# Kernel tuning notes

Measured on AMD Instinct MI355X. Metric: run time of the kernel, lower is better.

The kernel has to match this reference:

```python
import jax, jax.numpy as jnp
import numpy as np

B, T, D = 2, 2048, 1024
H, KVH = 16, 4
HD = D // H            # 64
HALF = HD // 2         # 32
DFF = 4096
KW = 15
EPS = 1e-6


def zcrms(x, scale):
    # zero-centred RMSNorm: (1 + scale) * x / rms(x)
    rms = jnp.sqrt(jnp.mean(jnp.square(x.astype(jnp.float32)), axis=-1, keepdims=True) + EPS)
    return ((1.0 + scale) * x / rms).astype(x.dtype)


def apply_rope(x, cos, sin):
    # x: [B, H, T, HD]; cos/sin: [T, HALF]
    c = cos[None, None, :, :]
    s = sin[None, None, :, :]
    x1, x2 = x[..., :HALF], x[..., HALF:]
    return jnp.concatenate([x1 * c - x2 * s, x2 * c + x1 * s], axis=-1)


def setup_inputs() -> dict:
    key = jax.random.key(0)
    ks = jax.random.split(key, 20)
    std = 0.02
    inp = {
        "x": jax.random.normal(ks[0], (B, T, D), jnp.float32),
        "mask": jnp.ones((1, 1, T, T), dtype=bool),
        "cos": jnp.cos(jnp.arange(T, dtype=jnp.float32)[:, None]
                       * (10000.0 ** (-jnp.arange(HALF, dtype=jnp.float32) / HALF))[None, :]),
        "sin": jnp.sin(jnp.arange(T, dtype=jnp.float32)[:, None]
                       * (10000.0 ** (-jnp.arange(HALF, dtype=jnp.float32) / HALF))[None, :]),
        # attention
        "attn_norm_scale": jax.random.normal(ks[1], (D,), jnp.float32) * std,
        "q_kernel": jax.random.normal(ks[2], (D, D), jnp.float32) * std,
        "k_kernel": jax.random.normal(ks[3], (D, KVH * HD), jnp.float32) * std,
        "v_kernel": jax.random.normal(ks[4], (D, KVH * HD), jnp.float32) * std,
        "q_norm_scale": jax.random.normal(ks[5], (HD,), jnp.float32) * std,
        "k_norm_scale": jax.random.normal(ks[6], (HD,), jnp.float32) * std,
        "o_kernel": jax.random.normal(ks[7], (D, D), jnp.float32) * std,
        # conv module
        "conv_norm_scale": jax.random.normal(ks[8], (D,), jnp.float32) * std,
        "pw_up_kernel": jax.random.normal(ks[9], (D, 2 * D), jnp.float32) * std,
        "dw_kernel": jax.random.normal(ks[10], (KW, 1, D), jnp.float32) * std,
        "conv_inner_norm_scale": jax.random.normal(ks[11], (D,), jnp.float32) * std,
        "pw_down_kernel": jax.random.normal(ks[12], (D, D), jnp.float32) * std,
        # ffn
        "ffn_norm_scale": jax.random.normal(ks[13], (D,), jnp.float32) * std,
        "gate_kernel": jax.random.normal(ks[14], (D, DFF), jnp.float32) * std,
        "up_kernel": jax.random.normal(ks[15], (D, DFF), jnp.float32) * std,
        "down_kernel": jax.random.normal(ks[16], (DFF, D), jnp.float32) * std,
    }
    return inp


def reference(x, mask, cos, sin, attn_norm_scale, q_kernel, k_kernel, v_kernel,
              q_norm_scale, k_norm_scale, o_kernel, conv_norm_scale, pw_up_kernel,
              dw_kernel, conv_inner_norm_scale, pw_down_kernel, ffn_norm_scale,
              gate_kernel, up_kernel, down_kernel):
    # ---- pre-norm self-attention (GQA + QK-RMSNorm + RoPE) ----
    h = zcrms(x, attn_norm_scale)
    q = (h @ q_kernel).reshape(B, T, H, HD).transpose(0, 2, 1, 3)      # [B,H,T,HD]
    k = (h @ k_kernel).reshape(B, T, KVH, HD).transpose(0, 2, 1, 3)    # [B,KVH,T,HD]
    v = (h @ v_kernel).reshape(B, T, KVH, HD).transpose(0, 2, 1, 3)
    q = zcrms(q, q_norm_scale)
    k = zcrms(k, k_norm_scale)
    rep = H // KVH
    k = jnp.repeat(k, rep, axis=1)
    v = jnp.repeat(v, rep, axis=1)
    q = apply_rope(q, cos, sin)
    k = apply_rope(k, cos, sin)
    scale = jnp.sqrt(jnp.float32(HD))
    aw = jnp.einsum('bhqd,bhkd->bhqk', q, k) / scale
    aw = jnp.where(mask, aw, jnp.finfo(aw.dtype).min)
    aw = jax.nn.softmax(aw, axis=-1)
    attn = jnp.einsum('bhqk,bhkd->bhqd', aw, v).transpose(0, 2, 1, 3).reshape(B, T, D)
    x = x + attn @ o_kernel

    # ---- conformer conv module: pw_up -> GLU -> depthwise conv -> norm -> pw_down ----
    h = zcrms(x, conv_norm_scale)
    u = h @ pw_up_kernel
    u1, u2 = jnp.split(u, 2, axis=-1)
    g = u1 * jax.nn.sigmoid(u2)                                        # [B,T,D]
    c = jax.lax.conv_general_dilated(
        g, dw_kernel, window_strides=(1,), padding='SAME',
        feature_group_count=D, dimension_numbers=('NWC', 'WIO', 'NWC'))
    c = zcrms(c, conv_inner_norm_scale)
    x = x + c @ pw_down_kernel

    # ---- gated FFN with drelu activation ----
    h = zcrms(x, ffn_norm_scale)
    ff = jax.nn.relu(h @ gate_kernel) * jax.nn.relu(h @ up_kernel)
    x = x + ff @ down_kernel
    return x
```

## Files before the change

kernel.cpp:

```cpp
#include <hip/hip_runtime.h>


#define TT   2048
#define NTOK 4096

typedef __attribute__((ext_vector_type(8))) short short8;
typedef __attribute__((ext_vector_type(4))) float floatx4;

__device__ __forceinline__ unsigned short f2bf(float f) {
  unsigned int u = __float_as_uint(f);
  u = (u + 0x7fffu + ((u >> 16) & 1u)) >> 16;
  return (unsigned short)u;
}
__device__ __forceinline__ float bf2f(unsigned short s) {
  return __uint_as_float(((unsigned int)s) << 16);
}

__device__ __forceinline__ void glds16(const void* g, void* lds_base) {
  __builtin_amdgcn_global_load_lds(
      (const __attribute__((address_space(1))) void*)g,
      (__attribute__((address_space(3))) void*)lds_base, 16, 0, 0);
}

__global__ void wconv_kernel(const float* __restrict__ src,
                             unsigned short* __restrict__ dst, int K, int M) {
  __shared__ float tile[32][33];
  int m0 = blockIdx.x * 32, k0 = blockIdx.y * 32;
  int tx = threadIdx.x, ty = threadIdx.y;
  for (int j = ty; j < 32; j += 8)
    tile[j][tx] = src[(size_t)(k0 + j) * M + (m0 + tx)];
  __syncthreads();
  for (int j = ty; j < 32; j += 8)
    dst[(size_t)(m0 + j) * K + (k0 + tx)] = f2bf(tile[tx][j]);
}

__global__ __launch_bounds__(256) void rmsnorm_kernel(
    const float* __restrict__ x, const float* __restrict__ scale,
    unsigned short* __restrict__ out) {
  int t = blockIdx.x, tid = threadIdx.x;
  float4 xv = ((const float4*)(x + (size_t)t * 1024))[tid];
  float ss = xv.x * xv.x + xv.y * xv.y + xv.z * xv.z + xv.w * xv.w;
#pragma unroll
  for (int off = 32; off > 0; off >>= 1) ss += __shfl_down(ss, off);
  __shared__ float red[4];
  if ((tid & 63) == 0) red[tid >> 6] = ss;
  __syncthreads();
  float rinv = rsqrtf((red[0] + red[1] + red[2] + red[3]) * (1.0f / 1024.0f) + 1e-6f);
  float4 sv = ((const float4*)scale)[tid];
  ushort4 o;
  o.x = f2bf((1.0f + sv.x) * xv.x * rinv);
  o.y = f2bf((1.0f + sv.y) * xv.y * rinv);
  o.z = f2bf((1.0f + sv.z) * xv.z * rinv);
  o.w = f2bf((1.0f + sv.w) * xv.w * rinv);
  ((ushort4*)(out + (size_t)t * 1024))[tid] = o;
}

template <int BN, bool OUT_BF16, bool RELU, bool RESID>
__global__ __launch_bounds__(256, 2) void gemm_bt_kernel(
    const unsigned short* __restrict__ A, const unsigned short* __restrict__ Bt,
    void* __restrict__ Cout, const float* __restrict__ resid, int K, int M) {
  constexpr int NI = BN / 32;
  __shared__ __align__(16) unsigned short As[128 * 64];
  __shared__ __align__(16) unsigned short Bs[BN * 64];
  const int tid = threadIdx.x;
  const int wid = tid >> 6, lane = tid & 63;
  const int quad = lane >> 4, l16 = lane & 15;
  const int wm = (wid >> 1) * 64, wn = (wid & 1) * (BN / 2);
  const int row0 = blockIdx.y * 128;
  const int col0 = blockIdx.x * BN;

  floatx4 acc[4][NI];
#pragma unroll
  for (int mi = 0; mi < 4; mi++)
#pragma unroll
    for (int ni = 0; ni < NI; ni++) acc[mi][ni] = (floatx4){0.f, 0.f, 0.f, 0.f};

  const unsigned short* Ag = A + (size_t)row0 * K;
  const unsigned short* Bg = Bt + (size_t)col0 * K;

  for (int k0 = 0; k0 < K; k0 += 64) {
#pragma unroll
    for (int j = 0; j < 4; j++) {
      int ci = tid + j * 256;
      int r = ci >> 3, c = (ci & 7) ^ (r & 7);
      glds16(Ag + (size_t)r * K + k0 + c * 8, &As[(wid * 64 + j * 256) * 8]);
    }
#pragma unroll
    for (int j = 0; j < BN / 32; j++) {
      int ci = tid + j * 256;
      int r = ci >> 3, c = (ci & 7) ^ (r & 7);
      glds16(Bg + (size_t)r * K + k0 + c * 8, &Bs[(wid * 64 + j * 256) * 8]);
    }
    __syncthreads();
#pragma unroll
    for (int kk = 0; kk < 64; kk += 32) {
      short8 a[4], b[NI];
#pragma unroll
      for (int mi = 0; mi < 4; mi++) {
        int r = wm + mi * 16 + l16;
        a[mi] = *(const short8*)&As[r * 64 + (((kk >> 3) + quad) ^ (r & 7)) * 8];
      }
#pragma unroll
      for (int ni = 0; ni < NI; ni++) {
        int r = wn + ni * 16 + l16;
        b[ni] = *(const short8*)&Bs[r * 64 + (((kk >> 3) + quad) ^ (r & 7)) * 8];
      }
#pragma unroll
      for (int mi = 0; mi < 4; mi++)
#pragma unroll
        for (int ni = 0; ni < NI; ni++)
          acc[mi][ni] = __builtin_amdgcn_mfma_f32_16x16x32_bf16(a[mi], b[ni], acc[mi][ni], 0, 0, 0);
    }
    __syncthreads();
  }
#pragma unroll
  for (int mi = 0; mi < 4; mi++) {
#pragma unroll
    for (int reg = 0; reg < 4; reg++) {
      int grow = row0 + wm + mi * 16 + quad * 4 + reg;
#pragma unroll
      for (int ni = 0; ni < NI; ni++) {
        int gcol = col0 + wn + ni * 16 + l16;
        float v = acc[mi][ni][reg];
        if (RESID) v += resid[(size_t)grow * M + gcol];
        if (RELU) v = fmaxf(v, 0.f);
        if (OUT_BF16) ((unsigned short*)Cout)[(size_t)grow * M + gcol] = f2bf(v);
        else          ((float*)Cout)[(size_t)grow * M + gcol] = v;
      }
    }
  }
}

#define QSCALE 0.180336880111f

__global__ __launch_bounds__(256) void qknorm_rope_kernel(
    const float* __restrict__ qkv, const float* __restrict__ cosb,
    const float* __restrict__ sinb, const float* __restrict__ qns,
    const float* __restrict__ kns, unsigned short* __restrict__ qb,
    unsigned short* __restrict__ kb, unsigned short* __restrict__ vb) {
  int tok = blockIdx.x;
  int tid = threadIdx.x, w = tid >> 6, lane = tid & 63;
  int pos = tok & (TT - 1);
  int half = lane & 31;
  float c = cosb[pos * 32 + half], s = sinb[pos * 32 + half];
  const float* row = qkv + (size_t)tok * 1536;
  for (int hr = w; hr < 20; hr += 4) {
    float v = row[hr * 64 + lane];
    float ss = v * v;
#pragma unroll
    for (int off = 32; off > 0; off >>= 1) ss += __shfl_xor(ss, off);
    float rinv = rsqrtf(ss * (1.0f / 64.0f) + 1e-6f);
    float sc = (hr < 16) ? qns[lane] : kns[lane];
    float nv = (1.0f + sc) * v * rinv;
    float partner = __shfl_xor(nv, 32);
    float outv = (lane < 32) ? (nv * c - partner * s) : (nv * c + partner * s);
    if (hr < 16) qb[(size_t)tok * 1024 + hr * 64 + lane] = f2bf(outv * QSCALE);
    else         kb[(size_t)tok * 256 + (hr - 16) * 64 + lane] = f2bf(outv);
  }
  vb[(size_t)tok * 256 + tid] = f2bf(row[1280 + tid]);
}

__global__ __launch_bounds__(256) void flash_kernel(
    const unsigned short* __restrict__ qb, const unsigned short* __restrict__ kb,
    const unsigned short* __restrict__ vb, unsigned short* __restrict__ ob) {
  int qt = blockIdx.x;
  int bh = blockIdx.y;
  int bi = bh >> 4, h = bh & 15, kvh = h >> 2;
  int tid = threadIdx.x, w = tid >> 6, lane = tid & 63;
  int quad = lane >> 4, l16 = lane & 15;

  __shared__ __align__(16) unsigned short Ks[2][64 * 64];
  __shared__ __align__(16) unsigned short Vt[2][64 * 72];
  __shared__ __align__(16) unsigned short Ps[64 * 76];

  const unsigned short* qsrc = qb + ((size_t)(bi * TT + qt * 64)) * 1024 + h * 64;
  short8 qf0 = *(const short8*)(qsrc + (size_t)(w * 16 + l16) * 1024 + quad * 8);
  short8 qf1 = *(const short8*)(qsrc + (size_t)(w * 16 + l16) * 1024 + 32 + quad * 8);

  const unsigned short* kbase = kb + ((size_t)(bi * TT)) * 256 + kvh * 64;
  const unsigned short* vbase = vb + ((size_t)(bi * TT)) * 256 + kvh * 64;

  floatx4 oacc[4];
  floatx4 lacc = (floatx4){0.f, 0.f, 0.f, 0.f};
#pragma unroll
  for (int i = 0; i < 4; i++) oacc[i] = (floatx4){0.f, 0.f, 0.f, 0.f};
  const short8 ones = (short8){0x3F80, 0x3F80, 0x3F80, 0x3F80,
                               0x3F80, 0x3F80, 0x3F80, 0x3F80};

  const int vkey = tid & 63, vd0 = (tid >> 6) * 8;

#pragma unroll
  for (int j = 0; j < 2; j++) {
    int ci = tid + j * 256;
    int r = ci >> 3, c = (ci & 7) ^ (r & 7);
    glds16(kbase + (size_t)r * 256 + c * 8, &Ks[0][(w * 64 + j * 256) * 8]);
  }
  {
    uint4 t0 = *(const uint4*)(vbase + (size_t)vkey * 256 + vd0);
    uint4 t1 = *(const uint4*)(vbase + (size_t)vkey * 256 + vd0 + 32);
    union { uint4 v; unsigned short u[8]; } uu;
    uu.v = t0;
#pragma unroll
    for (int e = 0; e < 8; e++) Vt[0][(vd0 + e) * 72 + vkey] = uu.u[e];
    uu.v = t1;
#pragma unroll
    for (int e = 0; e < 8; e++) Vt[0][(vd0 + 32 + e) * 72 + vkey] = uu.u[e];
  }

  for (int kt = 0; kt < 32; kt++) {
    const int bufi = kt & 1;
    __syncthreads();
    uint4 n0 = {0, 0, 0, 0}, n1 = {0, 0, 0, 0};
    if (kt < 31) {
#pragma unroll
      for (int j = 0; j < 2; j++) {
        int ci = tid + j * 256;
        int r = ci >> 3, c = (ci & 7) ^ (r & 7);
        glds16(kbase + (size_t)((kt + 1) * 64 + r) * 256 + c * 8,
               &Ks[bufi ^ 1][(w * 64 + j * 256) * 8]);
      }
      n0 = *(const uint4*)(vbase + (size_t)((kt + 1) * 64 + vkey) * 256 + vd0);
      n1 = *(const uint4*)(vbase + (size_t)((kt + 1) * 64 + vkey) * 256 + vd0 + 32);
    }

    float p[4][4];
#pragma unroll
    for (int ni = 0; ni < 4; ni++) {
      int rb = ni * 16 + l16;
      short8 b0 = *(const short8*)&Ks[bufi][rb * 64 + (quad ^ (rb & 7)) * 8];
      short8 b1 = *(const short8*)&Ks[bufi][rb * 64 + ((4 + quad) ^ (rb & 7)) * 8];
      floatx4 s = (floatx4){0.f, 0.f, 0.f, 0.f};
      s = __builtin_amdgcn_mfma_f32_16x16x32_bf16(qf0, b0, s, 0, 0, 0);
      s = __builtin_amdgcn_mfma_f32_16x16x32_bf16(qf1, b1, s, 0, 0, 0);
#pragma unroll
      for (int r = 0; r < 4; r++) p[ni][r] = __builtin_amdgcn_exp2f(s[r]);
    }
#pragma unroll
    for (int ni = 0; ni < 4; ni++)
#pragma unroll
      for (int r = 0; r < 4; r++)
        Ps[(w * 16 + quad * 4 + r) * 76 + ni * 16 + l16] =
            (unsigned short)(__float_as_uint(p[ni][r]) >> 16);
    short8 pa0 = *(const short8*)&Ps[(w * 16 + l16) * 76 + quad * 8];
    short8 pa1 = *(const short8*)&Ps[(w * 16 + l16) * 76 + 32 + quad * 8];
    lacc = __builtin_amdgcn_mfma_f32_16x16x32_bf16(pa0, ones, lacc, 0, 0, 0);
    lacc = __builtin_amdgcn_mfma_f32_16x16x32_bf16(pa1, ones, lacc, 0, 0, 0);
#pragma unroll
    for (int di = 0; di < 4; di++) {
      short8 b0 = *(const short8*)&Vt[bufi][(di * 16 + l16) * 72 + quad * 8];
      short8 b1 = *(const short8*)&Vt[bufi][(di * 16 + l16) * 72 + 32 + quad * 8];
      oacc[di] = __builtin_amdgcn_mfma_f32_16x16x32_bf16(pa0, b0, oacc[di], 0, 0, 0);
      oacc[di] = __builtin_amdgcn_mfma_f32_16x16x32_bf16(pa1, b1, oacc[di], 0, 0, 0);
    }

    if (kt < 31) {
      union { uint4 v; unsigned short u[8]; } uu;
      uu.v = n0;
#pragma unroll
      for (int e = 0; e < 8; e++) Vt[bufi ^ 1][(vd0 + e) * 72 + vkey] = uu.u[e];
      uu.v = n1;
#pragma unroll
      for (int e = 0; e < 8; e++) Vt[bufi ^ 1][(vd0 + 32 + e) * 72 + vkey] = uu.u[e];
    }
  }

  unsigned short* obase = ob + ((size_t)(bi * TT + qt * 64)) * 1024 + h * 64;
  float rl[4];
#pragma unroll
  for (int r = 0; r < 4; r++) rl[r] = 1.0f / lacc[r];
#pragma unroll
  for (int di = 0; di < 4; di++)
#pragma unroll
    for (int r = 0; r < 4; r++) {
      int qrow = w * 16 + quad * 4 + r;
      obase[(size_t)qrow * 1024 + di * 16 + l16] = f2bf(oacc[di][r] * rl[r]);
    }
}

__global__ __launch_bounds__(256) void glu_kernel(const float* __restrict__ u,
                                                  unsigned short* __restrict__ g) {
  int idx = blockIdx.x * 256 + threadIdx.x;
  int t = idx >> 8, c4 = (idx & 255) * 4;
  float4 a = *(const float4*)(u + (size_t)t * 2048 + c4);
  float4 b = *(const float4*)(u + (size_t)t * 2048 + 1024 + c4);
  ushort4 o;
  o.x = f2bf(a.x / (1.0f + __expf(-b.x)));
  o.y = f2bf(a.y / (1.0f + __expf(-b.y)));
  o.z = f2bf(a.z / (1.0f + __expf(-b.z)));
  o.w = f2bf(a.w / (1.0f + __expf(-b.w)));
  *(ushort4*)(g + (size_t)t * 1024 + c4) = o;
}

__global__ __launch_bounds__(256) void convnorm_kernel(
    const unsigned short* __restrict__ g, const float* __restrict__ dw,
    const float* __restrict__ scale, unsigned short* __restrict__ out) {
  int tok = blockIdx.x;
  int bi = tok >> 11, pos = tok & (TT - 1);
  int tid = threadIdx.x, c0 = tid * 4;
  float a0 = 0.f, a1 = 0.f, a2 = 0.f, a3 = 0.f;
#pragma unroll
  for (int wk = 0; wk < 15; wk++) {
    int pp = pos + wk - 7;
    if (pp < 0 || pp >= TT) continue;
    ushort4 gv = *(const ushort4*)(g + ((size_t)(bi * TT + pp)) * 1024 + c0);
    float4 kv = *(const float4*)(dw + wk * 1024 + c0);
    a0 += bf2f(gv.x) * kv.x;
    a1 += bf2f(gv.y) * kv.y;
    a2 += bf2f(gv.z) * kv.z;
    a3 += bf2f(gv.w) * kv.w;
  }
  float ss = a0 * a0 + a1 * a1 + a2 * a2 + a3 * a3;
#pragma unroll
  for (int off = 32; off > 0; off >>= 1) ss += __shfl_down(ss, off);
  __shared__ float red[4];
  if ((tid & 63) == 0) red[tid >> 6] = ss;
  __syncthreads();
  float rinv = rsqrtf((red[0] + red[1] + red[2] + red[3]) * (1.0f / 1024.0f) + 1e-6f);
  float4 sv = *(const float4*)(scale + c0);
  ushort4 o;
  o.x = f2bf((1.0f + sv.x) * a0 * rinv);
  o.y = f2bf((1.0f + sv.y) * a1 * rinv);
  o.z = f2bf((1.0f + sv.z) * a2 * rinv);
  o.w = f2bf((1.0f + sv.w) * a3 * rinv);
  *(ushort4*)(out + (size_t)tok * 1024 + c0) = o;
}

__global__ __launch_bounds__(256) void ffmul_kernel(
    const unsigned short* __restrict__ gu, unsigned short* __restrict__ ff) {
  int idx = blockIdx.x * 256 + threadIdx.x;
  int t = idx >> 10, c4 = (idx & 1023) * 4;
  ushort4 a = *(const ushort4*)(gu + (size_t)t * 8192 + c4);
  ushort4 b = *(const ushort4*)(gu + (size_t)t * 8192 + 4096 + c4);
  ushort4 o;
  o.x = f2bf(bf2f(a.x) * bf2f(b.x));
  o.y = f2bf(bf2f(a.y) * bf2f(b.y));
  o.z = f2bf(bf2f(a.z) * bf2f(b.z));
  o.w = f2bf(bf2f(a.w) * bf2f(b.w));
  *(ushort4*)(ff + (size_t)t * 4096 + c4) = o;
}

extern "C" void kernel_launch(void* const* d_in, const int* in_sizes, int n_in,
                              void* d_out, int out_size, void* d_ws, size_t ws_size,
                              hipStream_t stream) {
  const float* x        = (const float*)d_in[0];
  const float* cosb     = (const float*)d_in[2];
  const float* sinb     = (const float*)d_in[3];
  const float* attn_ns  = (const float*)d_in[4];
  const float* qkern    = (const float*)d_in[5];
  const float* kkern    = (const float*)d_in[6];
  const float* vkern    = (const float*)d_in[7];
  const float* qns      = (const float*)d_in[8];
  const float* kns      = (const float*)d_in[9];
  const float* okern    = (const float*)d_in[10];
  const float* conv_ns  = (const float*)d_in[11];
  const float* pwupk    = (const float*)d_in[12];
  const float* dwk      = (const float*)d_in[13];
  const float* convi_ns = (const float*)d_in[14];
  const float* pwdnk    = (const float*)d_in[15];
  const float* ffn_ns   = (const float*)d_in[16];
  const float* gatek    = (const float*)d_in[17];
  const float* upk      = (const float*)d_in[18];
  const float* downk    = (const float*)d_in[19];
  float* out = (float*)d_out;
  char* ws = (char*)d_ws;

  const size_t O_QKVT = 0;
  const size_t O_OT   = O_QKVT + (size_t)1536 * 1024 * 2;
  const size_t O_UPT  = O_OT   + (size_t)1024 * 1024 * 2;
  const size_t O_DNT  = O_UPT  + (size_t)2048 * 1024 * 2;
  const size_t O_GUT  = O_DNT  + (size_t)1024 * 1024 * 2;
  const size_t O_DWNT = O_GUT  + (size_t)8192 * 1024 * 2;
  const size_t O_H    = O_DWNT + (size_t)4096 * 1024 * 2;
  const size_t O_BIG1 = O_H    + (size_t)4096 * 1024 * 2;
  const size_t O_QB   = O_BIG1 + (size_t)4096 * 8192 * 2;
  const size_t O_KB   = O_QB   + (size_t)4096 * 1024 * 2;
  const size_t O_VB   = O_KB   + (size_t)4096 * 256 * 2;
  const size_t O_ECN  = O_VB   + (size_t)4096 * 256 * 2;
  const size_t O_X1   = O_ECN  + (size_t)4096 * 1024 * 2;
  const size_t O_X2   = O_X1   + (size_t)4096 * 1024 * 4;
  const size_t O_BIG2 = O_X2   + (size_t)4096 * 1024 * 4;

  unsigned short* qkvT = (unsigned short*)(ws + O_QKVT);
  unsigned short* oT   = (unsigned short*)(ws + O_OT);
  unsigned short* upT  = (unsigned short*)(ws + O_UPT);
  unsigned short* dnT  = (unsigned short*)(ws + O_DNT);
  unsigned short* guT  = (unsigned short*)(ws + O_GUT);
  unsigned short* dwT  = (unsigned short*)(ws + O_DWNT);
  unsigned short* hbuf = (unsigned short*)(ws + O_H);
  float*          big1f = (float*)(ws + O_BIG1);
  unsigned short* big1u = (unsigned short*)(ws + O_BIG1);
  unsigned short* qbuf = (unsigned short*)(ws + O_QB);
  unsigned short* kbuf = (unsigned short*)(ws + O_KB);
  unsigned short* vbuf = (unsigned short*)(ws + O_VB);
  unsigned short* ecn  = (unsigned short*)(ws + O_ECN);
  float*          x1   = (float*)(ws + O_X1);
  float*          x2   = (float*)(ws + O_X2);
  unsigned short* big2 = (unsigned short*)(ws + O_BIG2);

  dim3 tb(32, 8);
  wconv_kernel<<<dim3(32, 32), tb, 0, stream>>>(qkern, qkvT, 1024, 1024);
  wconv_kernel<<<dim3(8, 32), tb, 0, stream>>>(kkern, qkvT + (size_t)1024 * 1024, 1024, 256);
  wconv_kernel<<<dim3(8, 32), tb, 0, stream>>>(vkern, qkvT + (size_t)1280 * 1024, 1024, 256);
  wconv_kernel<<<dim3(32, 32), tb, 0, stream>>>(okern, oT, 1024, 1024);
  wconv_kernel<<<dim3(64, 32), tb, 0, stream>>>(pwupk, upT, 1024, 2048);
  wconv_kernel<<<dim3(32, 32), tb, 0, stream>>>(pwdnk, dnT, 1024, 1024);
  wconv_kernel<<<dim3(128, 32), tb, 0, stream>>>(gatek, guT, 1024, 4096);
  wconv_kernel<<<dim3(128, 32), tb, 0, stream>>>(upk, guT + (size_t)4096 * 1024, 1024, 4096);
  wconv_kernel<<<dim3(32, 128), tb, 0, stream>>>(downk, dwT, 4096, 1024);

  rmsnorm_kernel<<<NTOK, 256, 0, stream>>>(x, attn_ns, hbuf);
  gemm_bt_kernel<128, false, false, false><<<dim3(12, 32), 256, 0, stream>>>(
      hbuf, qkvT, big1f, nullptr, 1024, 1536);
  qknorm_rope_kernel<<<NTOK, 256, 0, stream>>>(big1f, cosb, sinb, qns, kns,
                                               qbuf, kbuf, vbuf);
  flash_kernel<<<dim3(32, 32), 256, 0, stream>>>(qbuf, kbuf, vbuf, ecn);
  gemm_bt_kernel<64, false, false, true><<<dim3(16, 32), 256, 0, stream>>>(
      ecn, oT, x1, x, 1024, 1024);

  rmsnorm_kernel<<<NTOK, 256, 0, stream>>>(x1, conv_ns, hbuf);
  gemm_bt_kernel<128, false, false, false><<<dim3(16, 32), 256, 0, stream>>>(
      hbuf, upT, big1f, nullptr, 1024, 2048);
  glu_kernel<<<4096, 256, 0, stream>>>(big1f, big2);
  convnorm_kernel<<<NTOK, 256, 0, stream>>>(big2, dwk, convi_ns, ecn);
  gemm_bt_kernel<64, false, false, true><<<dim3(16, 32), 256, 0, stream>>>(
      ecn, dnT, x2, x1, 1024, 1024);

  rmsnorm_kernel<<<NTOK, 256, 0, stream>>>(x2, ffn_ns, hbuf);
  gemm_bt_kernel<128, true, true, false><<<dim3(64, 32), 256, 0, stream>>>(
      hbuf, guT, big1u, nullptr, 1024, 8192);
  ffmul_kernel<<<16384, 256, 0, stream>>>(big1u, big2);
  gemm_bt_kernel<64, false, false, true><<<dim3(16, 32), 256, 0, stream>>>(
      big2, dwT, out, x2, 4096, 1024);
}
```

Measured before the change: 565.3 us.

## Batch weight conversions into one launch and restructure flash attention tiling

All nine weight transpose-and-convert launches are merged into a single kernel that reads a job table, cutting launch overhead. V is pre-transposed into a separate buffer by a new kernel, so flash attention can load V tiles straight into LDS with async swizzled copies instead of scattering through registers each iteration. Each flash block now handles 128 query rows (32 per wave), reusing every K/V tile across two MFMA row fragments, with a swizzled P buffer. The costs are an extra transpose kernel, more workspace, and half as many flash blocks (512), which may lower occupancy.

```diff
diff --git a/kernel.cpp b/kernel.cpp
--- a/kernel.cpp
+++ b/kernel.cpp
@@ -22,16 +22,30 @@
       (__attribute__((address_space(3))) void*)lds_base, 16, 0, 0);
 }
 
-__global__ void wconv_kernel(const float* __restrict__ src,
-                             unsigned short* __restrict__ dst, int K, int M) {
+struct WJobs {
+  const float* src[9];
+  unsigned short* dst[9];
+  int K[9], M[9];
+  int start[10];
+};
+
+__global__ __launch_bounds__(256) void wconv_all_kernel(WJobs tab) {
+  int b = blockIdx.x;
+  int j = 0;
+  while (b >= tab.start[j + 1]) j++;
+  int t = b - tab.start[j];
+  const float* src = tab.src[j];
+  unsigned short* dst = tab.dst[j];
+  int K = tab.K[j], M = tab.M[j];
+  int mt = M >> 5;
+  int m0 = (t % mt) * 32, k0 = (t / mt) * 32;
   __shared__ float tile[32][33];
-  int m0 = blockIdx.x * 32, k0 = blockIdx.y * 32;
-  int tx = threadIdx.x, ty = threadIdx.y;
-  for (int j = ty; j < 32; j += 8)
-    tile[j][tx] = src[(size_t)(k0 + j) * M + (m0 + tx)];
+  int tx = threadIdx.x & 31, ty = threadIdx.x >> 5;
+  for (int r = ty; r < 32; r += 8)
+    tile[r][tx] = src[(size_t)(k0 + r) * M + m0 + tx];
   __syncthreads();
-  for (int j = ty; j < 32; j += 8)
-    dst[(size_t)(m0 + j) * K + (k0 + tx)] = f2bf(tile[tx][j]);
+  for (int r = ty; r < 32; r += 8)
+    dst[(size_t)(m0 + r) * K + k0 + tx] = f2bf(tile[tx][r]);
 }
 
 __global__ __launch_bounds__(256) void rmsnorm_kernel(
@@ -160,121 +174,150 @@
   vb[(size_t)tok * 256 + tid] = f2bf(row[1280 + tid]);
 }
 
+__global__ __launch_bounds__(256) void vtrans_kernel(
+    const unsigned short* __restrict__ vb, unsigned short* __restrict__ vt) {
+  __shared__ unsigned short t[64 * 65];
+  int ktile = blockIdx.x;
+  int g = blockIdx.y;
+  int bi = g >> 2, kvh = g & 3;
+  int tid = threadIdx.x;
+#pragma unroll
+  for (int j = 0; j < 2; j++) {
+    int ci = tid + j * 256;
+    int r = ci >> 3, c8 = (ci & 7) * 8;
+    union { uint4 v; unsigned short u[8]; } uu;
+    uu.v = *(const uint4*)(vb + (size_t)(bi * TT + ktile * 64 + r) * 256 + kvh * 64 + c8);
+#pragma unroll
+    for (int e = 0; e < 8; e++) t[r * 65 + c8 + e] = uu.u[e];
+  }
+  __syncthreads();
+#pragma unroll
+  for (int j = 0; j < 2; j++) {
+    int ci = tid + j * 256;
+    int d = ci >> 3, c8 = (ci & 7) * 8;
+    union { uint4 v; unsigned short u[8]; } uu;
+#pragma unroll
+    for (int e = 0; e < 8; e++) uu.u[e] = t[(c8 + e) * 65 + d];
+    *(uint4*)(vt + ((size_t)(g * 64 + d)) * TT + ktile * 64 + c8) = uu.v;
+  }
+}
+
 __global__ __launch_bounds__(256) void flash_kernel(
     const unsigned short* __restrict__ qb, const unsigned short* __restrict__ kb,
-    const unsigned short* __restrict__ vb, unsigned short* __restrict__ ob) {
-  int qt = blockIdx.x;
-  int bh = blockIdx.y;
-  int bi = bh >> 4, h = bh & 15, kvh = h >> 2;
-  int tid = threadIdx.x, w = tid >> 6, lane = tid & 63;
-  int quad = lane >> 4, l16 = lane & 15;
+    const unsigned short* __restrict__ vt, unsigned short* __restrict__ ob) {
+  const int qt = blockIdx.x;
+  const int bh = blockIdx.y;
+  const int bi = bh >> 4, h = bh & 15, kvh = h >> 2;
+  const int tid = threadIdx.x, w = tid >> 6, lane = tid & 63;
+  const int quad = lane >> 4, l16 = lane & 15;
 
   __shared__ __align__(16) unsigned short Ks[2][64 * 64];
-  __shared__ __align__(16) unsigned short Vt[2][64 * 72];
-  __shared__ __align__(16) unsigned short Ps[64 * 76];
-
-  const unsigned short* qsrc = qb + ((size_t)(bi * TT + qt * 64)) * 1024 + h * 64;
-  short8 qf0 = *(const short8*)(qsrc + (size_t)(w * 16 + l16) * 1024 + quad * 8);
-  short8 qf1 = *(const short8*)(qsrc + (size_t)(w * 16 + l16) * 1024 + 32 + quad * 8);
+  __shared__ __align__(16) unsigned short Vs[2][64 * 64];
+  __shared__ __align__(16) unsigned short Ps[128 * 72];
+
+  const unsigned short* qsrc = qb + ((size_t)(bi * TT + qt * 128)) * 1024 + h * 64;
+  short8 qf[2][2];
+#pragma unroll
+  for (int af = 0; af < 2; af++) {
+    const unsigned short* qr = qsrc + (size_t)(w * 32 + af * 16 + l16) * 1024;
+    qf[af][0] = *(const short8*)(qr + quad * 8);
+    qf[af][1] = *(const short8*)(qr + 32 + quad * 8);
+  }
 
   const unsigned short* kbase = kb + ((size_t)(bi * TT)) * 256 + kvh * 64;
-  const unsigned short* vbase = vb + ((size_t)(bi * TT)) * 256 + kvh * 64;
-
-  floatx4 oacc[4];
-  floatx4 lacc = (floatx4){0.f, 0.f, 0.f, 0.f};
-#pragma unroll
-  for (int i = 0; i < 4; i++) oacc[i] = (floatx4){0.f, 0.f, 0.f, 0.f};
+  const unsigned short* vbase = vt + ((size_t)(bi * 4 + kvh)) * (64 * TT);
+
+  floatx4 oacc[2][4];
+  floatx4 lacc[2];
+#pragma unroll
+  for (int af = 0; af < 2; af++) {
+    lacc[af] = (floatx4){0.f, 0.f, 0.f, 0.f};
+#pragma unroll
+    for (int di = 0; di < 4; di++) oacc[af][di] = (floatx4){0.f, 0.f, 0.f, 0.f};
+  }
   const short8 ones = (short8){0x3F80, 0x3F80, 0x3F80, 0x3F80,
                                0x3F80, 0x3F80, 0x3F80, 0x3F80};
-
-  const int vkey = tid & 63, vd0 = (tid >> 6) * 8;
 
 #pragma unroll
   for (int j = 0; j < 2; j++) {
     int ci = tid + j * 256;
     int r = ci >> 3, c = (ci & 7) ^ (r & 7);
     glds16(kbase + (size_t)r * 256 + c * 8, &Ks[0][(w * 64 + j * 256) * 8]);
-  }
-  {
-    uint4 t0 = *(const uint4*)(vbase + (size_t)vkey * 256 + vd0);
-    uint4 t1 = *(const uint4*)(vbase + (size_t)vkey * 256 + vd0 + 32);
-    union { uint4 v; unsigned short u[8]; } uu;
-    uu.v = t0;
-#pragma unroll
-    for (int e = 0; e < 8; e++) Vt[0][(vd0 + e) * 72 + vkey] = uu.u[e];
-    uu.v = t1;
-#pragma unroll
-    for (int e = 0; e < 8; e++) Vt[0][(vd0 + 32 + e) * 72 + vkey] = uu.u[e];
+    glds16(vbase + (size_t)r * TT + c * 8, &Vs[0][(w * 64 + j * 256) * 8]);
   }
 
   for (int kt = 0; kt < 32; kt++) {
-    const int bufi = kt & 1;
+    const int buf = kt & 1;
     __syncthreads();
-    uint4 n0 = {0, 0, 0, 0}, n1 = {0, 0, 0, 0};
     if (kt < 31) {
 #pragma unroll
       for (int j = 0; j < 2; j++) {
         int ci = tid + j * 256;
         int r = ci >> 3, c = (ci & 7) ^ (r & 7);
         glds16(kbase + (size_t)((kt + 1) * 64 + r) * 256 + c * 8,
-               &Ks[bufi ^ 1][(w * 64 + j * 256) * 8]);
-      }
-      n0 = *(const uint4*)(vbase + (size_t)((kt + 1) * 64 + vkey) * 256 + vd0);
-      n1 = *(const uint4*)(vbase + (size_t)((kt + 1) * 64 + vkey) * 256 + vd0 + 32);
-    }
-
-    float p[4][4];
+               &Ks[buf ^ 1][(w * 64 + j * 256) * 8]);
+        glds16(vbase + (size_t)r * TT + (kt + 1) * 64 + c * 8,
+               &Vs[buf ^ 1][(w * 64 + j * 256) * 8]);
+      }
+    }
+
+    short8 kf[4][2];
 #pragma unroll
     for (int ni = 0; ni < 4; ni++) {
       int rb = ni * 16 + l16;
-      short8 b0 = *(const short8*)&Ks[bufi][rb * 64 + (quad ^ (rb & 7)) * 8];
-      short8 b1 = *(const short8*)&Ks[bufi][rb * 64 + ((4 + quad) ^ (rb & 7)) * 8];
-      floatx4 s = (floatx4){0.f, 0.f, 0.f, 0.f};
-      s = __builtin_amdgcn_mfma_f32_16x16x32_bf16(qf0, b0, s, 0, 0, 0);
-      s = __builtin_amdgcn_mfma_f32_16x16x32_bf16(qf1, b1, s, 0, 0, 0);
-#pragma unroll
-      for (int r = 0; r < 4; r++) p[ni][r] = __builtin_amdgcn_exp2f(s[r]);
-    }
-#pragma unroll
-    for (int ni = 0; ni < 4; ni++)
-#pragma unroll
-      for (int r = 0; r < 4; r++)
-        Ps[(w * 16 + quad * 4 + r) * 76 + ni * 16 + l16] =
-            (unsigned short)(__float_as_uint(p[ni][r]) >> 16);
-    short8 pa0 = *(const short8*)&Ps[(w * 16 + l16) * 76 + quad * 8];
-    short8 pa1 = *(const short8*)&Ps[(w * 16 + l16) * 76 + 32 + quad * 8];
-    lacc = __builtin_amdgcn_mfma_f32_16x16x32_bf16(pa0, ones, lacc, 0, 0, 0);
-    lacc = __builtin_amdgcn_mfma_f32_16x16x32_bf16(pa1, ones, lacc, 0, 0, 0);
+      kf[ni][0] = *(const short8*)&Ks[buf][rb * 64 + ((quad ^ (rb & 7)) * 8)];
+      kf[ni][1] = *(const short8*)&Ks[buf][rb * 64 + (((4 + quad) ^ (rb & 7)) * 8)];
+    }
+#pragma unroll
+    for (int af = 0; af < 2; af++) {
+#pragma unroll
+      for (int ni = 0; ni < 4; ni++) {
+        floatx4 s = (floatx4){0.f, 0.f, 0.f, 0.f};
+        s = __builtin_amdgcn_mfma_f32_16x16x32_bf16(qf[af][0], kf[ni][0], s, 0, 0, 0);
+        s = __builtin_amdgcn_mfma_f32_16x16x32_bf16(qf[af][1], kf[ni][1], s, 0, 0, 0);
+#pragma unroll
+        for (int r = 0; r < 4; r++)
+          Ps[(w * 32 + af * 16 + quad * 4 + r) * 72 + ((ni ^ quad) * 16 + l16)] =
+              (unsigned short)(__float_as_uint(__builtin_amdgcn_exp2f(s[r])) >> 16);
+      }
+    }
+    short8 vf[4][2];
 #pragma unroll
     for (int di = 0; di < 4; di++) {
-      short8 b0 = *(const short8*)&Vt[bufi][(di * 16 + l16) * 72 + quad * 8];
-      short8 b1 = *(const short8*)&Vt[bufi][(di * 16 + l16) * 72 + 32 + quad * 8];
-      oacc[di] = __builtin_amdgcn_mfma_f32_16x16x32_bf16(pa0, b0, oacc[di], 0, 0, 0);
-      oacc[di] = __builtin_amdgcn_mfma_f32_16x16x32_bf16(pa1, b1, oacc[di], 0, 0, 0);
-    }
-
-    if (kt < 31) {
-      union { uint4 v; unsigned short u[8]; } uu;
-      uu.v = n0;
-#pragma unroll
-      for (int e = 0; e < 8; e++) Vt[bufi ^ 1][(vd0 + e) * 72 + vkey] = uu.u[e];
-      uu.v = n1;
-#pragma unroll
-      for (int e = 0; e < 8; e++) Vt[bufi ^ 1][(vd0 + 32 + e) * 72 + vkey] = uu.u[e];
-    }
-  }
-
-  unsigned short* obase = ob + ((size_t)(bi * TT + qt * 64)) * 1024 + h * 64;
-  float rl[4];
-#pragma unroll
-  for (int r = 0; r < 4; r++) rl[r] = 1.0f / lacc[r];
-#pragma unroll
-  for (int di = 0; di < 4; di++)
-#pragma unroll
-    for (int r = 0; r < 4; r++) {
-      int qrow = w * 16 + quad * 4 + r;
-      obase[(size_t)qrow * 1024 + di * 16 + l16] = f2bf(oacc[di][r] * rl[r]);
-    }
+      int rb = di * 16 + l16;
+      vf[di][0] = *(const short8*)&Vs[buf][rb * 64 + ((quad ^ (rb & 7)) * 8)];
+      vf[di][1] = *(const short8*)&Vs[buf][rb * 64 + (((4 + quad) ^ (rb & 7)) * 8)];
+    }
+#pragma unroll
+    for (int af = 0; af < 2; af++) {
+      const int rr = w * 32 + af * 16 + l16;
+      const int sw = l16 >> 2;
+      short8 pa0 = *(const short8*)&Ps[rr * 72 + (((quad >> 1) ^ sw) * 16 + (quad & 1) * 8)];
+      short8 pa1 = *(const short8*)&Ps[rr * 72 + ((((quad >> 1) + 2) ^ sw) * 16 + (quad & 1) * 8)];
+      lacc[af] = __builtin_amdgcn_mfma_f32_16x16x32_bf16(pa0, ones, lacc[af], 0, 0, 0);
+      lacc[af] = __builtin_amdgcn_mfma_f32_16x16x32_bf16(pa1, ones, lacc[af], 0, 0, 0);
+#pragma unroll
+      for (int di = 0; di < 4; di++) {
+        oacc[af][di] = __builtin_amdgcn_mfma_f32_16x16x32_bf16(pa0, vf[di][0], oacc[af][di], 0, 0, 0);
+        oacc[af][di] = __builtin_amdgcn_mfma_f32_16x16x32_bf16(pa1, vf[di][1], oacc[af][di], 0, 0, 0);
+      }
+    }
+  }
+
+  unsigned short* obase = ob + ((size_t)(bi * TT + qt * 128)) * 1024 + h * 64;
+#pragma unroll
+  for (int af = 0; af < 2; af++) {
+    float rl[4];
+#pragma unroll
+    for (int r = 0; r < 4; r++) rl[r] = 1.0f / lacc[af][r];
+#pragma unroll
+    for (int di = 0; di < 4; di++)
+#pragma unroll
+      for (int r = 0; r < 4; r++) {
+        int qrow = w * 32 + af * 16 + quad * 4 + r;
+        obase[(size_t)qrow * 1024 + di * 16 + l16] = f2bf(oacc[af][di][r] * rl[r]);
+      }
+  }
 }
 
 __global__ __launch_bounds__(256) void glu_kernel(const float* __restrict__ u,
@@ -375,7 +418,8 @@
   const size_t O_QB   = O_BIG1 + (size_t)4096 * 8192 * 2;
   const size_t O_KB   = O_QB   + (size_t)4096 * 1024 * 2;
   const size_t O_VB   = O_KB   + (size_t)4096 * 256 * 2;
-  const size_t O_ECN  = O_VB   + (size_t)4096 * 256 * 2;
+  const size_t O_VT   = O_VB   + (size_t)4096 * 256 * 2;
+  const size_t O_ECN  = O_VT   + (size_t)8 * 64 * 2048 * 2;
   const size_t O_X1   = O_ECN  + (size_t)4096 * 1024 * 2;
   const size_t O_X2   = O_X1   + (size_t)4096 * 1024 * 4;
   const size_t O_BIG2 = O_X2   + (size_t)4096 * 1024 * 4;
@@ -392,28 +436,34 @@
   unsigned short* qbuf = (unsigned short*)(ws + O_QB);
   unsigned short* kbuf = (unsigned short*)(ws + O_KB);
   unsigned short* vbuf = (unsigned short*)(ws + O_VB);
+  unsigned short* vtb  = (unsigned short*)(ws + O_VT);
   unsigned short* ecn  = (unsigned short*)(ws + O_ECN);
   float*          x1   = (float*)(ws + O_X1);
   float*          x2   = (float*)(ws + O_X2);
   unsigned short* big2 = (unsigned short*)(ws + O_BIG2);
 
-  dim3 tb(32, 8);
-  wconv_kernel<<<dim3(32, 32), tb, 0, stream>>>(qkern, qkvT, 1024, 1024);
-  wconv_kernel<<<dim3(8, 32), tb, 0, stream>>>(kkern, qkvT + (size_t)1024 * 1024, 1024, 256);
-  wconv_kernel<<<dim3(8, 32), tb, 0, stream>>>(vkern, qkvT + (size_t)1280 * 1024, 1024, 256);
-  wconv_kernel<<<dim3(32, 32), tb, 0, stream>>>(okern, oT, 1024, 1024);
-  wconv_kernel<<<dim3(64, 32), tb, 0, stream>>>(pwupk, upT, 1024, 2048);
-  wconv_kernel<<<dim3(32, 32), tb, 0, stream>>>(pwdnk, dnT, 1024, 1024);
-  wconv_kernel<<<dim3(128, 32), tb, 0, stream>>>(gatek, guT, 1024, 4096);
-  wconv_kernel<<<dim3(128, 32), tb, 0, stream>>>(upk, guT + (size_t)4096 * 1024, 1024, 4096);
-  wconv_kernel<<<dim3(32, 128), tb, 0, stream>>>(downk, dwT, 4096, 1024);
+  WJobs tab;
+  tab.src[0] = qkern;  tab.dst[0] = qkvT;                         tab.K[0] = 1024; tab.M[0] = 1024;
+  tab.src[1] = kkern;  tab.dst[1] = qkvT + (size_t)1024 * 1024;   tab.K[1] = 1024; tab.M[1] = 256;
+  tab.src[2] = vkern;  tab.dst[2] = qkvT + (size_t)1280 * 1024;   tab.K[2] = 1024; tab.M[2] = 256;
+  tab.src[3] = okern;  tab.dst[3] = oT;                           tab.K[3] = 1024; tab.M[3] = 1024;
+  tab.src[4] = pwupk;  tab.dst[4] = upT;                          tab.K[4] = 1024; tab.M[4] = 2048;
+  tab.src[5] = pwdnk;  tab.dst[5] = dnT;                          tab.K[5] = 1024; tab.M[5] = 1024;
+  tab.src[6] = gatek;  tab.dst[6] = guT;                          tab.K[6] = 1024; tab.M[6] = 4096;
+  tab.src[7] = upk;    tab.dst[7] = guT + (size_t)4096 * 1024;    tab.K[7] = 1024; tab.M[7] = 4096;
+  tab.src[8] = downk;  tab.dst[8] = dwT;                          tab.K[8] = 4096; tab.M[8] = 1024;
+  tab.start[0] = 0;
+  for (int i = 0; i < 9; i++)
+    tab.start[i + 1] = tab.start[i] + (tab.M[i] >> 5) * (tab.K[i] >> 5);
+  wconv_all_kernel<<<tab.start[9], 256, 0, stream>>>(tab);
 
   rmsnorm_kernel<<<NTOK, 256, 0, stream>>>(x, attn_ns, hbuf);
   gemm_bt_kernel<128, false, false, false><<<dim3(12, 32), 256, 0, stream>>>(
       hbuf, qkvT, big1f, nullptr, 1024, 1536);
   qknorm_rope_kernel<<<NTOK, 256, 0, stream>>>(big1f, cosb, sinb, qns, kns,
                                                qbuf, kbuf, vbuf);
-  flash_kernel<<<dim3(32, 32), 256, 0, stream>>>(qbuf, kbuf, vbuf, ecn);
+  vtrans_kernel<<<dim3(32, 8), 256, 0, stream>>>(vbuf, vtb);
+  flash_kernel<<<dim3(16, 32), 256, 0, stream>>>(qbuf, kbuf, vtb, ecn);
   gemm_bt_kernel<64, false, false, true><<<dim3(16, 32), 256, 0, stream>>>(
       ecn, oT, x1, x, 1024, 1024);
 
```

Result: faster. 516.4 us (-8.7%).
